# Optimization experiments

Hardware: AMD Instinct MI355X
Metric: run time of the kernel (lower is better)

## Reference

```python
import jax, jax.numpy as jnp
import numpy as np

T = 8_000_000
S_INIT = 0.5  # module init kwarg S_init
B_INIT = 1.0  # module init kwarg B_init


def setup_inputs() -> dict:
    key = jax.random.key(0)
    x = jax.random.uniform(key, (T, 2), dtype=jnp.float32)  # [:,0]=precip, [:,1]=evap
    # Learned params, shape (1,) as in flax setup(), at their constant() init values.
    BFI = jnp.full((1,), 0.5, dtype=jnp.float32)
    K = jnp.full((1,), 0.5, dtype=jnp.float32)
    S_max = jnp.full((1,), 1.0, dtype=jnp.float32)
    return {"x": x, "BFI": BFI, "K": K, "S_max": S_max}


def _awbm_scan(x, bfi, k, smax):
    # Sequential AWBM bucket update. The original uses lax.cond(S>S_max, excess, noexcess);
    # both branches coincide exactly when excess = max(S - S_max, 0) == 0, so a select
    # form computes identical math without the cond.
    def step(carry, xt):
        S, B = carry
        S = jnp.maximum(S + xt[0] - xt[1], 0.0)          # relu(S + precip - evap)
        excess = jnp.maximum(S - smax, 0.0)
        S = S - excess                                    # clamp store to S_max on excess
        outflow = (1.0 - bfi) * excess
        B = B + bfi * excess
        baseflow = (1.0 - k) * B
        B = B - baseflow
        totalflow = outflow + baseflow
        return (S, B), totalflow.reshape((1,))

    carry0 = (jnp.float32(S_INIT), jnp.float32(B_INIT))
    _, totalflow = jax.lax.scan(step, carry0, x)
    return totalflow  # [T, 1]


def reference(x, BFI, K, S_max):
    return _awbm_scan(x, BFI[0], K[0], S_max[0])
```

## Files before the change

kernel.cpp:

```cpp
#include <hip/hip_runtime.h>

constexpr int TPB   = 256;
constexpr int ITEMS = 31;
constexpr int TILE  = TPB * ITEMS;
constexpr int GRID  = 1024;
constexpr unsigned MAGIC = 0xC0DE600Du;


#define AT_LOAD(p)    __hip_atomic_load((p), __ATOMIC_RELAXED, __HIP_MEMORY_SCOPE_AGENT)
#define AT_STORE(p,v) __hip_atomic_store((p), (v), __ATOMIC_RELAXED, __HIP_MEMORY_SCOPE_AGENT)

__global__ __launch_bounds__(TPB, 4)
void awbm_kernel(const float* __restrict__ x,
                 const float* __restrict__ pBFI,
                 const float* __restrict__ pK,
                 const float* __restrict__ pSmax,
                 float* __restrict__ out,
                 float* __restrict__ ws,
                 int T)
{
    __shared__ __align__(16) float lds_d[TILE];
    __shared__ float sm[12];
    __shared__ unsigned svid;

    const int tid  = threadIdx.x;
    const int lane = tid & 63;
    const int wv   = tid >> 6;

    float*    scrA   = ws;
    float*    scrB   = ws + GRID;
    float*    scrC   = ws + 2 * GRID;
    float*    scrP   = ws + 3 * GRID;
    float*    scrQ   = ws + 4 * GRID;
    unsigned* f1     = (unsigned*)(ws + 5 * GRID);
    unsigned* f2     = (unsigned*)(ws + 6 * GRID);
    unsigned* ticket = (unsigned*)(ws + 7 * GRID);

    if (tid == 0)
        svid = __hip_atomic_fetch_add(ticket, 1u, __ATOMIC_RELAXED, __HIP_MEMORY_SCOPE_AGENT);

    const float bfi  = pBFI[0];
    const float k    = pK[0];
    const float smax = pSmax[0];
    const float omb  = 1.0f - bfi;
    const float omk  = 1.0f - k;
    const float INF  = __builtin_inff();

    __syncthreads();
    const int b     = (int)svid;
    const int gbase = b * TILE;

    {
        const float4* x4 = (const float4*)x;
        float2* d2 = (float2*)lds_d;
        for (int i = tid; i < TILE / 2; i += TPB) {
            int e = gbase + 2 * i;
            float2 dv; dv.x = 0.f; dv.y = 0.f;
            if (e < T) {
                float4 v = x4[(gbase >> 1) + i];
                dv.x = v.x - v.y;
                dv.y = v.z - v.w;
            }
            d2[i] = dv;
        }
    }
    __syncthreads();

    const int toff = tid * ITEMS;
    int m = T - gbase - toff;
    m = m < 0 ? 0 : (m > ITEMS ? ITEMS : m);

    float rA = 0.f, rB = -INF, rC = INF;
    if (m == ITEMS) {
#pragma unroll
        for (int j = 0; j < ITEMS; ++j) {
            float d = lds_d[toff + j];
            rA += d;
            rB = fmaxf(rB + d, 0.f);
            rC = fminf(fmaxf(rC + d, 0.f), smax);
        }
    } else {
        for (int j = 0; j < m; ++j) {
            float d = lds_d[toff + j];
            rA += d;
            rB = fmaxf(rB + d, 0.f);
            rC = fminf(fmaxf(rC + d, 0.f), smax);
        }
    }
#pragma unroll
    for (int s = 1; s < 64; s <<= 1) {
        float pA = __shfl_up(rA, s, 64), pB = __shfl_up(rB, s, 64), pC = __shfl_up(rC, s, 64);
        if (lane >= s) {
            float nA = pA + rA, nB = fmaxf(pB + rA, rB), nC = fminf(fmaxf(pC + rA, rB), rC);
            rA = nA; rB = nB; rC = nC;
        }
    }
    if (lane == 63) { sm[wv * 3] = rA; sm[wv * 3 + 1] = rB; sm[wv * 3 + 2] = rC; }
    __syncthreads();
    float wA = 0.f, wB = -INF, wC = INF;
    for (int i = 0; i < wv; ++i) {
        float a = sm[i * 3], bb = sm[i * 3 + 1], c = sm[i * 3 + 2];
        float nA = wA + a, nB = fmaxf(wB + a, bb), nC = fminf(fmaxf(wC + a, bb), c);
        wA = nA; wB = nB; wC = nC;
    }
    {
        float nA = wA + rA, nB = fmaxf(wB + rA, rB), nC = fminf(fmaxf(wC + rA, rB), rC);
        rA = nA; rB = nB; rC = nC;
    }
    if (tid == TPB - 1) {
        AT_STORE(&scrA[b], rA); AT_STORE(&scrB[b], rB); AT_STORE(&scrC[b], rC);
        __atomic_signal_fence(__ATOMIC_SEQ_CST);
        __builtin_amdgcn_s_waitcnt(0);
        __atomic_signal_fence(__ATOMIC_SEQ_CST);
        AT_STORE(&f1[b], MAGIC);
    }
    float eA, eB, eC;
    {
        float pA = __shfl_up(rA, 1, 64), pB = __shfl_up(rB, 1, 64), pC = __shfl_up(rC, 1, 64);
        eA = (lane == 0) ? wA : pA;
        eB = (lane == 0) ? wB : pB;
        eC = (lane == 0) ? wC : pC;
    }

    const int base4 = 4 * tid;
    unsigned need = 0;
#pragma unroll
    for (int q = 0; q < 4; ++q) if (base4 + q < b) need |= (1u << q);
    {
        unsigned pend = need;
        while (pend) {
            unsigned got = 0;
#pragma unroll
            for (int q = 0; q < 4; ++q)
                if ((pend >> q) & 1u)
                    if (AT_LOAD(&f1[base4 + q]) == MAGIC) got |= (1u << q);
            pend &= ~got;
            if (pend) __builtin_amdgcn_s_sleep(1);
        }
    }
    __atomic_signal_fence(__ATOMIC_ACQUIRE);
    float cA = 0.f, cB = -INF, cC = INF;
#pragma unroll
    for (int q = 0; q < 4; ++q) {
        if ((need >> q) & 1u) {
            float ga = AT_LOAD(&scrA[base4 + q]);
            float gb = AT_LOAD(&scrB[base4 + q]);
            float gc = AT_LOAD(&scrC[base4 + q]);
            float nA = cA + ga, nB = fmaxf(cB + ga, gb), nC = fminf(fmaxf(cC + ga, gb), gc);
            cA = nA; cB = nB; cC = nC;
        }
    }
#pragma unroll
    for (int s = 1; s < 64; s <<= 1) {
        float oa = __shfl_down(cA, s, 64), ob = __shfl_down(cB, s, 64), oc = __shfl_down(cC, s, 64);
        float nA = cA + oa, nB = fmaxf(cB + oa, ob), nC = fminf(fmaxf(cC + oa, ob), oc);
        cA = nA; cB = nB; cC = nC;
    }
    __syncthreads();
    if (lane == 0) { sm[wv * 3] = cA; sm[wv * 3 + 1] = cB; sm[wv * 3 + 2] = cC; }
    __syncthreads();
    float S;
    {
        float FA = 0.f, FB = -INF, FC = INF;
        for (int i = 0; i < 4; ++i) {
            float a = sm[i * 3], bb = sm[i * 3 + 1], c = sm[i * 3 + 2];
            float nA = FA + a, nB = fmaxf(FB + a, bb), nC = fminf(fmaxf(FC + a, bb), c);
            FA = nA; FB = nB; FC = nC;
        }
        S = fminf(fmaxf(0.5f + FA, FB), FC);
        S = fminf(fmaxf(S + eA, eB), eC);
    }

    float p = 1.f, c = 0.f;
    if (m == ITEMS) {
#pragma unroll
        for (int j = 0; j < ITEMS; ++j) {
            float d  = lds_d[toff + j];
            float S1 = fmaxf(S + d, 0.f);
            float ex = fmaxf(S1 - smax, 0.f);
            S = S1 - ex;
            float w = c + bfi * ex;
            lds_d[toff + j] = omb * ex + omk * w;
            c = k * w;
            p *= k;
        }
    } else {
        for (int j = 0; j < m; ++j) {
            float d  = lds_d[toff + j];
            float S1 = fmaxf(S + d, 0.f);
            float ex = fmaxf(S1 - smax, 0.f);
            S = S1 - ex;
            float w = c + bfi * ex;
            lds_d[toff + j] = omb * ex + omk * w;
            c = k * w;
            p *= k;
        }
    }
#pragma unroll
    for (int s = 1; s < 64; s <<= 1) {
        float pp = __shfl_up(p, s, 64), pc = __shfl_up(c, s, 64);
        if (lane >= s) {
            float nq = p * pc + c;
            p = pp * p;
            c = nq;
        }
    }
    __syncthreads();
    if (lane == 63) { sm[wv * 2] = p; sm[wv * 2 + 1] = c; }
    __syncthreads();
    float wP = 1.f, wQ = 0.f;
    for (int i = 0; i < wv; ++i) {
        float gp = sm[i * 2], gq = sm[i * 2 + 1];
        wQ = gp * wQ + gq;
        wP = wP * gp;
    }
    {
        float nq = p * wQ + c;
        p = wP * p;
        c = nq;
    }
    if (tid == TPB - 1) {
        AT_STORE(&scrP[b], p); AT_STORE(&scrQ[b], c);
        __atomic_signal_fence(__ATOMIC_SEQ_CST);
        __builtin_amdgcn_s_waitcnt(0);
        __atomic_signal_fence(__ATOMIC_SEQ_CST);
        AT_STORE(&f2[b], MAGIC);
    }
    float eP, eQ;
    {
        float pp = __shfl_up(p, 1, 64), pc = __shfl_up(c, 1, 64);
        eP = (lane == 0) ? wP : pp;
        eQ = (lane == 0) ? wQ : pc;
    }

    {
        unsigned pend = need;
        while (pend) {
            unsigned got = 0;
#pragma unroll
            for (int q = 0; q < 4; ++q)
                if ((pend >> q) & 1u)
                    if (AT_LOAD(&f2[base4 + q]) == MAGIC) got |= (1u << q);
            pend &= ~got;
            if (pend) __builtin_amdgcn_s_sleep(1);
        }
    }
    __atomic_signal_fence(__ATOMIC_ACQUIRE);
    float cP = 1.f, cQ = 0.f;
#pragma unroll
    for (int q = 0; q < 4; ++q) {
        if ((need >> q) & 1u) {
            float gp = AT_LOAD(&scrP[base4 + q]);
            float gq = AT_LOAD(&scrQ[base4 + q]);
            cQ = gp * cQ + gq;
            cP = cP * gp;
        }
    }
#pragma unroll
    for (int s = 1; s < 64; s <<= 1) {
        float op = __shfl_down(cP, s, 64), oq = __shfl_down(cQ, s, 64);
        float nq = op * cQ + oq;
        cP = cP * op;
        cQ = nq;
    }
    __syncthreads();
    if (lane == 0) { sm[wv * 2] = cP; sm[wv * 2 + 1] = cQ; }
    __syncthreads();
    float Bst;
    {
        float FP = 1.f, FQ = 0.f;
        for (int i = 0; i < 4; ++i) {
            float gp = sm[i * 2], gq = sm[i * 2 + 1];
            FQ = gp * FQ + gq;
            FP = FP * gp;
        }
        Bst = FP * 1.0f + FQ;
        Bst = eP * Bst + eQ;
    }

    float f = omk * Bst;
    if (m == ITEMS) {
#pragma unroll
        for (int j = 0; j < ITEMS; ++j) { lds_d[toff + j] += f; f *= k; }
    } else {
        for (int j = 0; j < m; ++j) { lds_d[toff + j] += f; f *= k; }
    }
    __syncthreads();
    {
        float4* out4 = (float4*)out;
        const float4* l4 = (const float4*)lds_d;
        for (int i = tid; i < TILE / 4; i += TPB) {
            int e = gbase + 4 * i;
            if (e < T) out4[(gbase >> 2) + i] = l4[i];
        }
    }
}

extern "C" void kernel_launch(void* const* d_in, const int* in_sizes, int n_in,
                              void* d_out, int out_size, void* d_ws, size_t ws_size,
                              hipStream_t stream) {
    const float* x    = (const float*)d_in[0];
    const float* BFI  = (const float*)d_in[1];
    const float* K    = (const float*)d_in[2];
    const float* Smax = (const float*)d_in[3];
    float* out = (float*)d_out;
    float* ws  = (float*)d_ws;
    int T = out_size;

    hipMemsetAsync((char*)d_ws + 7 * GRID * sizeof(float), 0, sizeof(unsigned), stream);
    awbm_kernel<<<dim3(GRID), dim3(TPB), 0, stream>>>(x, BFI, K, Smax, out, ws, T);
}
```

Measured before the change: 141.7 us.

## Use global completion counters and single-wave lookback, cache tile in registers

Each block now bumps a global counter after publishing its aggregate. One wave in every consumer block waits on that counter before checking the per-block flags, which replaces polling spread across all four waves. Partial aggregates are packed into 64-bit stores, and the final reduction runs in a single wave, so the cross-wave LDS combine and one barrier are gone. Each thread keeps its 31 items in registers between passes to cut LDS traffic, at the cost of higher register pressure. Counter waiting adds serialization and more atomic traffic on one address.

After: 229.8 us. 62.2% more time.

```diff
diff --git a/kernel.cpp b/kernel.cpp
--- a/kernel.cpp
+++ b/kernel.cpp
@@ -9,6 +9,14 @@
 
 #define AT_LOAD(p)    __hip_atomic_load((p), __ATOMIC_RELAXED, __HIP_MEMORY_SCOPE_AGENT)
 #define AT_STORE(p,v) __hip_atomic_store((p), (v), __ATOMIC_RELAXED, __HIP_MEMORY_SCOPE_AGENT)
+
+__device__ __forceinline__ unsigned long long pack2(float a, float b) {
+    union { float f[2]; unsigned long long u; } v; v.f[0] = a; v.f[1] = b; return v.u;
+}
+__device__ __forceinline__ float2 unpack2(unsigned long long u) {
+    union { float f[2]; unsigned long long u; } v; v.u = u;
+    return make_float2(v.f[0], v.f[1]);
+}
 
 __global__ __launch_bounds__(TPB, 4)
 void awbm_kernel(const float* __restrict__ x,
@@ -20,24 +28,24 @@
                  int T)
 {
     __shared__ __align__(16) float lds_d[TILE];
-    __shared__ float sm[12];
+    __shared__ float sm3[12];
+    __shared__ float sm2[8];
+    __shared__ float bc[5];
     __shared__ unsigned svid;
 
     const int tid  = threadIdx.x;
     const int lane = tid & 63;
     const int wv   = tid >> 6;
 
-    float*    scrA   = ws;
-    float*    scrB   = ws + GRID;
-    float*    scrC   = ws + 2 * GRID;
-    float*    scrP   = ws + 3 * GRID;
-    float*    scrQ   = ws + 4 * GRID;
-    unsigned* f1     = (unsigned*)(ws + 5 * GRID);
-    unsigned* f2     = (unsigned*)(ws + 6 * GRID);
-    unsigned* ticket = (unsigned*)(ws + 7 * GRID);
+    unsigned long long* scrAB1 = (unsigned long long*)ws;
+    float*              scrC1  = (float*)((char*)ws + 8192);
+    unsigned long long* scrPQ2 = (unsigned long long*)((char*)ws + 12288);
+    unsigned*           f1     = (unsigned*)((char*)ws + 20480);
+    unsigned*           f2     = (unsigned*)((char*)ws + 24576);
+    unsigned*           ctrl   = (unsigned*)((char*)ws + 28672);
 
     if (tid == 0)
-        svid = __hip_atomic_fetch_add(ticket, 1u, __ATOMIC_RELAXED, __HIP_MEMORY_SCOPE_AGENT);
+        svid = __hip_atomic_fetch_add(&ctrl[0], 1u, __ATOMIC_RELAXED, __HIP_MEMORY_SCOPE_AGENT);
 
     const float bfi  = pBFI[0];
     const float k    = pK[0];
@@ -69,12 +77,15 @@
     const int toff = tid * ITEMS;
     int m = T - gbase - toff;
     m = m < 0 ? 0 : (m > ITEMS ? ITEMS : m);
-
+    const bool full = (m == ITEMS);
+
+    float dreg[ITEMS];
     float rA = 0.f, rB = -INF, rC = INF;
-    if (m == ITEMS) {
+    if (full) {
 #pragma unroll
         for (int j = 0; j < ITEMS; ++j) {
             float d = lds_d[toff + j];
+            dreg[j] = d;
             rA += d;
             rB = fmaxf(rB + d, 0.f);
             rC = fminf(fmaxf(rC + d, 0.f), smax);
@@ -95,11 +106,11 @@
             rA = nA; rB = nB; rC = nC;
         }
     }
-    if (lane == 63) { sm[wv * 3] = rA; sm[wv * 3 + 1] = rB; sm[wv * 3 + 2] = rC; }
+    if (lane == 63) { sm3[wv * 3] = rA; sm3[wv * 3 + 1] = rB; sm3[wv * 3 + 2] = rC; }
     __syncthreads();
     float wA = 0.f, wB = -INF, wC = INF;
     for (int i = 0; i < wv; ++i) {
-        float a = sm[i * 3], bb = sm[i * 3 + 1], c = sm[i * 3 + 2];
+        float a = sm3[i * 3], bb = sm3[i * 3 + 1], c = sm3[i * 3 + 2];
         float nA = wA + a, nB = fmaxf(wB + a, bb), nC = fminf(fmaxf(wC + a, bb), c);
         wA = nA; wB = nB; wC = nC;
     }
@@ -108,11 +119,16 @@
         rA = nA; rB = nB; rC = nC;
     }
     if (tid == TPB - 1) {
-        AT_STORE(&scrA[b], rA); AT_STORE(&scrB[b], rB); AT_STORE(&scrC[b], rC);
+        AT_STORE(&scrAB1[b], pack2(rA, rB));
+        AT_STORE(&scrC1[b], rC);
         __atomic_signal_fence(__ATOMIC_SEQ_CST);
         __builtin_amdgcn_s_waitcnt(0);
         __atomic_signal_fence(__ATOMIC_SEQ_CST);
         AT_STORE(&f1[b], MAGIC);
+        __atomic_signal_fence(__ATOMIC_SEQ_CST);
+        __builtin_amdgcn_s_waitcnt(0);
+        __atomic_signal_fence(__ATOMIC_SEQ_CST);
+        __hip_atomic_fetch_add(&ctrl[1], 1u, __ATOMIC_RELAXED, __HIP_MEMORY_SCOPE_AGENT);
     }
     float eA, eB, eC;
     {
@@ -122,65 +138,51 @@
         eC = (lane == 0) ? wC : pC;
     }
 
-    const int base4 = 4 * tid;
-    unsigned need = 0;
-#pragma unroll
-    for (int q = 0; q < 4; ++q) if (base4 + q < b) need |= (1u << q);
-    {
-        unsigned pend = need;
+    if (wv == 0) {
+        if (lane == 0)
+            while ((int)AT_LOAD(&ctrl[1]) < b) __builtin_amdgcn_s_sleep(2);
+        const int s0 = lane * 16;
+        int cnt = b - s0; cnt = cnt < 0 ? 0 : (cnt > 16 ? 16 : cnt);
+        unsigned pend = (cnt >= 16) ? 0xFFFFu : ((1u << cnt) - 1u);
         while (pend) {
-            unsigned got = 0;
-#pragma unroll
-            for (int q = 0; q < 4; ++q)
-                if ((pend >> q) & 1u)
-                    if (AT_LOAD(&f1[base4 + q]) == MAGIC) got |= (1u << q);
-            pend &= ~got;
+            for (int j = 0; j < 16; ++j)
+                if ((pend >> j) & 1u)
+                    if (AT_LOAD(&f1[s0 + j]) == MAGIC) pend &= ~(1u << j);
             if (pend) __builtin_amdgcn_s_sleep(1);
         }
-    }
-    __atomic_signal_fence(__ATOMIC_ACQUIRE);
-    float cA = 0.f, cB = -INF, cC = INF;
-#pragma unroll
-    for (int q = 0; q < 4; ++q) {
-        if ((need >> q) & 1u) {
-            float ga = AT_LOAD(&scrA[base4 + q]);
-            float gb = AT_LOAD(&scrB[base4 + q]);
-            float gc = AT_LOAD(&scrC[base4 + q]);
-            float nA = cA + ga, nB = fmaxf(cB + ga, gb), nC = fminf(fmaxf(cC + ga, gb), gc);
+        __atomic_signal_fence(__ATOMIC_ACQUIRE);
+        float cA = 0.f, cB = -INF, cC = INF;
+        for (int j = 0; j < cnt; ++j) {
+            float2 ab = unpack2(AT_LOAD(&scrAB1[s0 + j]));
+            float  gc = AT_LOAD(&scrC1[s0 + j]);
+            float nA = cA + ab.x, nB = fmaxf(cB + ab.x, ab.y), nC = fminf(fmaxf(cC + ab.x, ab.y), gc);
             cA = nA; cB = nB; cC = nC;
         }
-    }
-#pragma unroll
-    for (int s = 1; s < 64; s <<= 1) {
-        float oa = __shfl_down(cA, s, 64), ob = __shfl_down(cB, s, 64), oc = __shfl_down(cC, s, 64);
-        float nA = cA + oa, nB = fmaxf(cB + oa, ob), nC = fminf(fmaxf(cC + oa, ob), oc);
-        cA = nA; cB = nB; cC = nC;
-    }
-    __syncthreads();
-    if (lane == 0) { sm[wv * 3] = cA; sm[wv * 3 + 1] = cB; sm[wv * 3 + 2] = cC; }
+#pragma unroll
+        for (int s = 1; s < 64; s <<= 1) {
+            float oa = __shfl_down(cA, s, 64), ob = __shfl_down(cB, s, 64), oc = __shfl_down(cC, s, 64);
+            float nA = cA + oa, nB = fmaxf(cB + oa, ob), nC = fminf(fmaxf(cC + oa, ob), oc);
+            cA = nA; cB = nB; cC = nC;
+        }
+        if (lane == 0) { bc[0] = cA; bc[1] = cB; bc[2] = cC; }
+    }
     __syncthreads();
     float S;
     {
-        float FA = 0.f, FB = -INF, FC = INF;
-        for (int i = 0; i < 4; ++i) {
-            float a = sm[i * 3], bb = sm[i * 3 + 1], c = sm[i * 3 + 2];
-            float nA = FA + a, nB = fmaxf(FB + a, bb), nC = fminf(fmaxf(FC + a, bb), c);
-            FA = nA; FB = nB; FC = nC;
-        }
-        S = fminf(fmaxf(0.5f + FA, FB), FC);
+        S = fminf(fmaxf(0.5f + bc[0], bc[1]), bc[2]);
         S = fminf(fmaxf(S + eA, eB), eC);
     }
 
     float p = 1.f, c = 0.f;
-    if (m == ITEMS) {
+    if (full) {
 #pragma unroll
         for (int j = 0; j < ITEMS; ++j) {
-            float d  = lds_d[toff + j];
+            float d  = dreg[j];
             float S1 = fmaxf(S + d, 0.f);
             float ex = fmaxf(S1 - smax, 0.f);
             S = S1 - ex;
             float w = c + bfi * ex;
-            lds_d[toff + j] = omb * ex + omk * w;
+            dreg[j] = omb * ex + omk * w;
             c = k * w;
             p *= k;
         }
@@ -205,12 +207,11 @@
             c = nq;
         }
     }
-    __syncthreads();
-    if (lane == 63) { sm[wv * 2] = p; sm[wv * 2 + 1] = c; }
+    if (lane == 63) { sm2[wv * 2] = p; sm2[wv * 2 + 1] = c; }
     __syncthreads();
     float wP = 1.f, wQ = 0.f;
     for (int i = 0; i < wv; ++i) {
-        float gp = sm[i * 2], gq = sm[i * 2 + 1];
+        float gp = sm2[i * 2], gq = sm2[i * 2 + 1];
         wQ = gp * wQ + gq;
         wP = wP * gp;
     }
@@ -220,11 +221,15 @@
         c = nq;
     }
     if (tid == TPB - 1) {
-        AT_STORE(&scrP[b], p); AT_STORE(&scrQ[b], c);
+        AT_STORE(&scrPQ2[b], pack2(p, c));
         __atomic_signal_fence(__ATOMIC_SEQ_CST);
         __builtin_amdgcn_s_waitcnt(0);
         __atomic_signal_fence(__ATOMIC_SEQ_CST);
         AT_STORE(&f2[b], MAGIC);
+        __atomic_signal_fence(__ATOMIC_SEQ_CST);
+        __builtin_amdgcn_s_waitcnt(0);
+        __atomic_signal_fence(__ATOMIC_SEQ_CST);
+        __hip_atomic_fetch_add(&ctrl[2], 1u, __ATOMIC_RELAXED, __HIP_MEMORY_SCOPE_AGENT);
     }
     float eP, eQ;
     {
@@ -233,55 +238,48 @@
         eQ = (lane == 0) ? wQ : pc;
     }
 
-    {
-        unsigned pend = need;
+    if (wv == 0) {
+        if (lane == 0)
+            while ((int)AT_LOAD(&ctrl[2]) < b) __builtin_amdgcn_s_sleep(2);
+        const int s0 = lane * 16;
+        int cnt = b - s0; cnt = cnt < 0 ? 0 : (cnt > 16 ? 16 : cnt);
+        unsigned pend = (cnt >= 16) ? 0xFFFFu : ((1u << cnt) - 1u);
         while (pend) {
-            unsigned got = 0;
-#pragma unroll
-            for (int q = 0; q < 4; ++q)
-                if ((pend >> q) & 1u)
-                    if (AT_LOAD(&f2[base4 + q]) == MAGIC) got |= (1u << q);
-            pend &= ~got;
+            for (int j = 0; j < 16; ++j)
+                if ((pend >> j) & 1u)
+                    if (AT_LOAD(&f2[s0 + j]) == MAGIC) pend &= ~(1u << j);
             if (pend) __builtin_amdgcn_s_sleep(1);
         }
-    }
-    __atomic_signal_fence(__ATOMIC_ACQUIRE);
-    float cP = 1.f, cQ = 0.f;
-#pragma unroll
-    for (int q = 0; q < 4; ++q) {
-        if ((need >> q) & 1u) {
-            float gp = AT_LOAD(&scrP[base4 + q]);
-            float gq = AT_LOAD(&scrQ[base4 + q]);
-            cQ = gp * cQ + gq;
-            cP = cP * gp;
-        }
-    }
-#pragma unroll
-    for (int s = 1; s < 64; s <<= 1) {
-        float op = __shfl_down(cP, s, 64), oq = __shfl_down(cQ, s, 64);
-        float nq = op * cQ + oq;
-        cP = cP * op;
-        cQ = nq;
-    }
-    __syncthreads();
-    if (lane == 0) { sm[wv * 2] = cP; sm[wv * 2 + 1] = cQ; }
+        __atomic_signal_fence(__ATOMIC_ACQUIRE);
+        float cP = 1.f, cQ = 0.f;
+        for (int j = 0; j < cnt; ++j) {
+            float2 pq = unpack2(AT_LOAD(&scrPQ2[s0 + j]));
+            cQ = pq.x * cQ + pq.y;
+            cP = cP * pq.x;
+        }
+#pragma unroll
+        for (int s = 1; s < 64; s <<= 1) {
+            float op = __shfl_down(cP, s, 64), oq = __shfl_down(cQ, s, 64);
+            float nq = op * cQ + oq;
+            cP = cP * op;
+            cQ = nq;
+        }
+        if (lane == 0) { bc[3] = cP; bc[4] = cQ; }
+    }
     __syncthreads();
     float Bst;
     {
-        float FP = 1.f, FQ = 0.f;
-        for (int i = 0; i < 4; ++i) {
-            float gp = sm[i * 2], gq = sm[i * 2 + 1];
-            FQ = gp * FQ + gq;
-            FP = FP * gp;
-        }
-        Bst = FP * 1.0f + FQ;
+        Bst = bc[3] * 1.0f + bc[4];
         Bst = eP * Bst + eQ;
     }
 
     float f = omk * Bst;
-    if (m == ITEMS) {
-#pragma unroll
-        for (int j = 0; j < ITEMS; ++j) { lds_d[toff + j] += f; f *= k; }
+    if (full) {
+#pragma unroll
+        for (int j = 0; j < ITEMS; ++j) {
+            lds_d[toff + j] = dreg[j] + f;
+            f *= k;
+        }
     } else {
         for (int j = 0; j < m; ++j) { lds_d[toff + j] += f; f *= k; }
     }
@@ -307,6 +305,6 @@
     float* ws  = (float*)d_ws;
     int T = out_size;
 
-    hipMemsetAsync((char*)d_ws + 7 * GRID * sizeof(float), 0, sizeof(unsigned), stream);
+    hipMemsetAsync((char*)d_ws + 28672, 0, 12, stream);
     awbm_kernel<<<dim3(GRID), dim3(TPB), 0, stream>>>(x, BFI, K, Smax, out, ws, T);
 }
```

## Replace full-prefix block aggregate scans with early-terminating single-thread lookback

Applied to the files above, without the earlier changes.

Each block previously waited on the flags of all preceding blocks and reduced their aggregates with a block-wide parallel scan. Now thread 0 walks backward through predecessor aggregates one at a time. It stops early once the clamp composition saturates (B >= C), or once the decay product underflows, then broadcasts the carry through shared memory. This removes the full dependence on every earlier block and the associated barriers. The cost is a serial walk and stricter chaining between neighbouring blocks, and the underflow cutoff is a small approximation.

Measured after the change: 127.5 us. 1.11x faster.

```diff
diff --git a/kernel.cpp b/kernel.cpp
--- a/kernel.cpp
+++ b/kernel.cpp
@@ -20,7 +20,9 @@
                  int T)
 {
     __shared__ __align__(16) float lds_d[TILE];
-    __shared__ float sm[12];
+    __shared__ float sm3[12];
+    __shared__ float sm2[8];
+    __shared__ float bc[2];
     __shared__ unsigned svid;
 
     const int tid  = threadIdx.x;
@@ -95,11 +97,11 @@
             rA = nA; rB = nB; rC = nC;
         }
     }
-    if (lane == 63) { sm[wv * 3] = rA; sm[wv * 3 + 1] = rB; sm[wv * 3 + 2] = rC; }
+    if (lane == 63) { sm3[wv * 3] = rA; sm3[wv * 3 + 1] = rB; sm3[wv * 3 + 2] = rC; }
     __syncthreads();
     float wA = 0.f, wB = -INF, wC = INF;
     for (int i = 0; i < wv; ++i) {
-        float a = sm[i * 3], bb = sm[i * 3 + 1], c = sm[i * 3 + 2];
+        float a = sm3[i * 3], bb = sm3[i * 3 + 1], c = sm3[i * 3 + 2];
         float nA = wA + a, nB = fmaxf(wB + a, bb), nC = fminf(fmaxf(wC + a, bb), c);
         wA = nA; wB = nB; wC = nC;
     }
@@ -122,54 +124,24 @@
         eC = (lane == 0) ? wC : pC;
     }
 
-    const int base4 = 4 * tid;
-    unsigned need = 0;
-#pragma unroll
-    for (int q = 0; q < 4; ++q) if (base4 + q < b) need |= (1u << q);
-    {
-        unsigned pend = need;
-        while (pend) {
-            unsigned got = 0;
-#pragma unroll
-            for (int q = 0; q < 4; ++q)
-                if ((pend >> q) & 1u)
-                    if (AT_LOAD(&f1[base4 + q]) == MAGIC) got |= (1u << q);
-            pend &= ~got;
-            if (pend) __builtin_amdgcn_s_sleep(1);
-        }
-    }
-    __atomic_signal_fence(__ATOMIC_ACQUIRE);
-    float cA = 0.f, cB = -INF, cC = INF;
-#pragma unroll
-    for (int q = 0; q < 4; ++q) {
-        if ((need >> q) & 1u) {
-            float ga = AT_LOAD(&scrA[base4 + q]);
-            float gb = AT_LOAD(&scrB[base4 + q]);
-            float gc = AT_LOAD(&scrC[base4 + q]);
-            float nA = cA + ga, nB = fmaxf(cB + ga, gb), nC = fminf(fmaxf(cC + ga, gb), gc);
-            cA = nA; cB = nB; cC = nC;
-        }
-    }
-#pragma unroll
-    for (int s = 1; s < 64; s <<= 1) {
-        float oa = __shfl_down(cA, s, 64), ob = __shfl_down(cB, s, 64), oc = __shfl_down(cC, s, 64);
-        float nA = cA + oa, nB = fmaxf(cB + oa, ob), nC = fminf(fmaxf(cC + oa, ob), oc);
-        cA = nA; cB = nB; cC = nC;
-    }
-    __syncthreads();
-    if (lane == 0) { sm[wv * 3] = cA; sm[wv * 3 + 1] = cB; sm[wv * 3 + 2] = cC; }
-    __syncthreads();
-    float S;
-    {
-        float FA = 0.f, FB = -INF, FC = INF;
-        for (int i = 0; i < 4; ++i) {
-            float a = sm[i * 3], bb = sm[i * 3 + 1], c = sm[i * 3 + 2];
-            float nA = FA + a, nB = fmaxf(FB + a, bb), nC = fminf(fmaxf(FC + a, bb), c);
-            FA = nA; FB = nB; FC = nC;
-        }
-        S = fminf(fmaxf(0.5f + FA, FB), FC);
-        S = fminf(fmaxf(S + eA, eB), eC);
-    }
+    if (tid == 0) {
+        float aA = 0.f, aB = -INF, aC = INF;
+        float Sst;
+        int j = b - 1;
+        for (;;) {
+            if (j < 0) { Sst = fminf(fmaxf(0.5f + aA, aB), aC); break; }
+            while (AT_LOAD(&f1[j]) != MAGIC) __builtin_amdgcn_s_sleep(1);
+            __atomic_signal_fence(__ATOMIC_ACQUIRE);
+            float Aj = AT_LOAD(&scrA[j]), Bj = AT_LOAD(&scrB[j]), Cj = AT_LOAD(&scrC[j]);
+            float nA = Aj + aA, nB = fmaxf(Bj + aA, aB), nC = fminf(fmaxf(Cj + aA, aB), aC);
+            aA = nA; aB = nB; aC = nC;
+            if (aB >= aC) { Sst = aC; break; }
+            --j;
+        }
+        bc[0] = Sst;
+    }
+    __syncthreads();
+    float S = fminf(fmaxf(bc[0] + eA, eB), eC);
 
     float p = 1.f, c = 0.f;
     if (m == ITEMS) {
@@ -205,12 +177,11 @@
             c = nq;
         }
     }
-    __syncthreads();
-    if (lane == 63) { sm[wv * 2] = p; sm[wv * 2 + 1] = c; }
+    if (lane == 63) { sm2[wv * 2] = p; sm2[wv * 2 + 1] = c; }
     __syncthreads();
     float wP = 1.f, wQ = 0.f;
     for (int i = 0; i < wv; ++i) {
-        float gp = sm[i * 2], gq = sm[i * 2 + 1];
+        float gp = sm2[i * 2], gq = sm2[i * 2 + 1];
         wQ = gp * wQ + gq;
         wP = wP * gp;
     }
@@ -233,50 +204,23 @@
         eQ = (lane == 0) ? wQ : pc;
     }
 
-    {
-        unsigned pend = need;
-        while (pend) {
-            unsigned got = 0;
-#pragma unroll
-            for (int q = 0; q < 4; ++q)
-                if ((pend >> q) & 1u)
-                    if (AT_LOAD(&f2[base4 + q]) == MAGIC) got |= (1u << q);
-            pend &= ~got;
-            if (pend) __builtin_amdgcn_s_sleep(1);
-        }
-    }
-    __atomic_signal_fence(__ATOMIC_ACQUIRE);
-    float cP = 1.f, cQ = 0.f;
-#pragma unroll
-    for (int q = 0; q < 4; ++q) {
-        if ((need >> q) & 1u) {
-            float gp = AT_LOAD(&scrP[base4 + q]);
-            float gq = AT_LOAD(&scrQ[base4 + q]);
-            cQ = gp * cQ + gq;
-            cP = cP * gp;
-        }
-    }
-#pragma unroll
-    for (int s = 1; s < 64; s <<= 1) {
-        float op = __shfl_down(cP, s, 64), oq = __shfl_down(cQ, s, 64);
-        float nq = op * cQ + oq;
-        cP = cP * op;
-        cQ = nq;
-    }
-    __syncthreads();
-    if (lane == 0) { sm[wv * 2] = cP; sm[wv * 2 + 1] = cQ; }
-    __syncthreads();
-    float Bst;
-    {
-        float FP = 1.f, FQ = 0.f;
-        for (int i = 0; i < 4; ++i) {
-            float gp = sm[i * 2], gq = sm[i * 2 + 1];
-            FQ = gp * FQ + gq;
-            FP = FP * gp;
-        }
-        Bst = FP * 1.0f + FQ;
-        Bst = eP * Bst + eQ;
-    }
+    if (tid == 0) {
+        float accP = 1.f, Bst = 0.f;
+        int j = b - 1;
+        for (;;) {
+            if (j < 0) { Bst += accP * 1.0f; break; }
+            if (accP < 1e-35f) break;
+            while (AT_LOAD(&f2[j]) != MAGIC) __builtin_amdgcn_s_sleep(1);
+            __atomic_signal_fence(__ATOMIC_ACQUIRE);
+            float Pj = AT_LOAD(&scrP[j]), Qj = AT_LOAD(&scrQ[j]);
+            Bst  += accP * Qj;
+            accP *= Pj;
+            --j;
+        }
+        bc[1] = Bst;
+    }
+    __syncthreads();
+    float Bst = eP * bc[1] + eQ;
 
     float f = omk * Bst;
     if (m == ITEMS) {
```
